# Kernel tuning notes

Measured on AMD Instinct MI355X. Metric: run time of the kernel, lower is better.

Reference implementation:

```python
import jax, jax.numpy as jnp
import numpy as np

EPS = 1e-5

def _quant_w(w):
    # symmetric per-tensor 8-bit weight quantization with straight-through estimator
    s = jnp.max(jnp.abs(w)) / 127.0
    wq = jnp.round(jnp.clip(w / s, -127.0, 127.0)) * s
    return w + jax.lax.stop_gradient(wq - w)

def _adder_conv(x, w, stride):
    # AdderNet conv: out[b,co,ow] = -sum_{cin,k} |x[b,cin,ow*stride+k] - w[co,cin,k]|
    # x: (B, Cin, L), w: (Co, Cin, K)
    B, Cin, L = x.shape
    Co, _, K = w.shape
    Ow = (L - K) // stride + 1
    idx = jnp.arange(Ow)[:, None] * stride + jnp.arange(K)[None, :]      # (Ow, K)
    patches = x[:, :, idx]                                               # (B, Cin, Ow, K)
    diff = jnp.abs(patches[:, None] - w[None, :, :, None, :])            # (B, Co, Cin, Ow, K)
    return -diff.sum(axis=(2, 4))                                        # (B, Co, Ow)

def _bn(x, p):
    # eval-mode BatchNorm; x: (B,C,W), p: (4,C) = [gamma, beta, running_mean, running_var]
    g, b, m, v = p
    return (x - m[:, None]) * (g[:, None] * jax.lax.rsqrt(v[:, None] + EPS)) + b[:, None]

def _bn_params(key, c):
    k1, k2, k3, k4 = jax.random.split(key, 4)
    g = jax.random.uniform(k1, (c,)) + 0.5
    b = 0.1 * jax.random.normal(k2, (c,))
    m = 0.1 * jax.random.normal(k3, (c,))
    v = jax.random.uniform(k4, (c,)) + 0.5
    return jnp.stack([g, b, m, v]).astype(jnp.float32)

def setup_inputs() -> dict:
    key = jax.random.key(0)
    ks = jax.random.split(key, 22)
    B = 8192
    w = lambda k, shp: (0.1 * jax.random.normal(k, shp)).astype(jnp.float32)
    return {
        'x': jax.random.normal(ks[0], (B, 1, 1, 256), dtype=jnp.float32),
        'w_pre1': w(ks[1], (5, 1, 13)),   'bn_pre1': _bn_params(ks[2], 5),
        'w_pre2': w(ks[3], (10, 5, 9)),   'bn_pre2': _bn_params(ks[4], 10),
        'w_r1':   w(ks[5], (10, 10, 1)),  'bn_r1':   _bn_params(ks[6], 10),
        'w_r2':   w(ks[7], (10, 10, 1)),  'bn_r2':   _bn_params(ks[8], 10),
        'w_o1a':  w(ks[9], (70, 140, 1)), 'bn_o1a':  _bn_params(ks[10], 70),
        'w_o1b':  w(ks[11], (30, 70, 1)), 'bn_o1b':  _bn_params(ks[12], 30),
        'w_o1c':  w(ks[13], (1, 30, 1)),  'bn_o1c':  _bn_params(ks[14], 1),
        'w_o2a':  w(ks[15], (70, 140, 1)),'bn_o2a':  _bn_params(ks[16], 70),
        'w_o2b':  w(ks[17], (30, 70, 1)), 'bn_o2b':  _bn_params(ks[18], 30),
        'w_o2c':  w(ks[19], (1, 30, 1)),  'bn_o2c':  _bn_params(ks[20], 1),
    }

def reference(x, w_pre1, bn_pre1, w_pre2, bn_pre2, w_r1, bn_r1, w_r2, bn_r2,
              w_o1a, bn_o1a, w_o1b, bn_o1b, w_o1c, bn_o1c,
              w_o2a, bn_o2a, w_o2b, bn_o2b, w_o2c, bn_o2c):
    relu = jax.nn.relu
    B = x.shape[0]
    h = x.reshape(B, 1, 256)                                  # height dim is 1 -> 1D
    h = relu(_bn(_adder_conv(h, _quant_w(w_pre1), 5), bn_pre1))   # (B,5,49)
    h = relu(_bn(_adder_conv(h, _quant_w(w_pre2), 3), bn_pre2))   # (B,10,14)
    # ResBlock
    t = relu(_bn(_adder_conv(h, _quant_w(w_r1), 1), bn_r1))
    t = _bn(_adder_conv(t, _quant_w(w_r2), 1), bn_r2)
    h = relu(t + h)                                           # (B,10,14)
    f = h.reshape(B, 140, 1)                                  # flatten to channels
    # O1 branch (amplitude-weighted average lifetime)
    a = relu(_bn(_adder_conv(f, _quant_w(w_o1a), 1), bn_o1a))
    a = relu(_bn(_adder_conv(a, _quant_w(w_o1b), 1), bn_o1b))
    a = relu(_bn(_adder_conv(a, _quant_w(w_o1c), 1), bn_o1c))
    tau_amp = a.reshape(-1)                                   # (B,)
    # O2 branch (intensity-weighted average lifetime)
    b = relu(_bn(_adder_conv(f, _quant_w(w_o2a), 1), bn_o2a))
    b = relu(_bn(_adder_conv(b, _quant_w(w_o2b), 1), bn_o2b))
    b = relu(_bn(_adder_conv(b, _quant_w(w_o2c), 1), bn_o2c))
    tau_inten = b.reshape(-1)                                 # (B,)
    return (tau_amp, tau_inten)
```

## Files before the change

kernel.cpp:

```cpp
#include <hip/hip_runtime.h>

#define TPB 256
#define EPB 8
#define H1S 246
#define ES  280

#define WQ1   0
#define WQ2   65
#define WR1Q  515
#define WR2Q  615
#define WCQ   715
#define WSB   779
#define SMALL_N 1253
#define WQAT  1280
#define WQBT  20880

#define SB_P1 0
#define SB_P2 10
#define SB_R1 30
#define SB_R2 50
#define SB_A1 70
#define SB_B1 210
#define SB_C1 270
#define SB_A2 272
#define SB_B2 412
#define SB_C2 472

#define GFOLD(bn, C, OFF)                                                     \
  if (tid < (C)) {                                                            \
    float gg = (bn)[tid], bb = (bn)[(C) + tid];                               \
    float mm = (bn)[2 * (C) + tid], vv = (bn)[3 * (C) + tid];                 \
    float sc = gg / sqrtf(vv + 1e-5f);                                        \
    sbp[(OFF) + tid] = sc;                                                    \
    sbp[(OFF) + (C) + tid] = bb - mm * sc;                                    \
  }

extern "C" __global__ __launch_bounds__(256)
void prep(const float* __restrict__ w1,  const float* __restrict__ bnp1,
          const float* __restrict__ w2,  const float* __restrict__ bnp2,
          const float* __restrict__ wr1, const float* __restrict__ bnr1,
          const float* __restrict__ wr2, const float* __restrict__ bnr2,
          const float* __restrict__ wa1, const float* __restrict__ bna1,
          const float* __restrict__ wb1, const float* __restrict__ bnb1,
          const float* __restrict__ wc1, const float* __restrict__ bnc1,
          const float* __restrict__ wa2, const float* __restrict__ bna2,
          const float* __restrict__ wb2, const float* __restrict__ bnb2,
          const float* __restrict__ wc2, const float* __restrict__ bnc2,
          float* __restrict__ ws)
{
  __shared__ float s_red[4];
  const int tid = threadIdx.x;
  const int b = blockIdx.x;

  if (b == 10) {
    float* sbp = ws + WSB;
    GFOLD(bnp1, 5, SB_P1)  GFOLD(bnp2, 10, SB_P2)
    GFOLD(bnr1, 10, SB_R1) GFOLD(bnr2, 10, SB_R2)
    GFOLD(bna1, 70, SB_A1) GFOLD(bnb1, 30, SB_B1) GFOLD(bnc1, 1, SB_C1)
    GFOLD(bna2, 70, SB_A2) GFOLD(bnb2, 30, SB_B2) GFOLD(bnc2, 1, SB_C2)
    return;
  }

  const float* src; int n; int mode; int rofs; float* dst = ws;
  int ofs = 0;
  switch (b) {
    case 0: src = w1;  ofs = WQ1;      n = 65;   mode = 0; rofs = 0;  break;
    case 1: src = w2;  ofs = WQ2;      n = 450;  mode = 0; rofs = 0;  break;
    case 2: src = wr1; ofs = WR1Q;     n = 100;  mode = 0; rofs = 0;  break;
    case 3: src = wr2; ofs = WR2Q;     n = 100;  mode = 0; rofs = 0;  break;
    case 4: src = wa1; ofs = WQAT;     n = 9800; mode = 1; rofs = 0;  break;
    case 5: src = wb1; ofs = WQBT;     n = 2100; mode = 2; rofs = 0;  break;
    case 6: src = wc1; ofs = WCQ;      n = 30;   mode = 0; rofs = 0;  break;
    case 7: src = wa2; ofs = WQAT;     n = 9800; mode = 1; rofs = 70; break;
    case 8: src = wb2; ofs = WQBT;     n = 2100; mode = 2; rofs = 30; break;
    default:src = wc2; ofs = WCQ + 32; n = 30;   mode = 0; rofs = 0;  break;
  }

  float m = 0.f;
  for (int i = tid; i < n; i += 256) m = fmaxf(m, fabsf(src[i]));
#pragma unroll
  for (int off = 32; off > 0; off >>= 1)
    m = fmaxf(m, __shfl_down(m, off, 64));
  if ((tid & 63) == 0) s_red[tid >> 6] = m;
  __syncthreads();
  m = fmaxf(fmaxf(s_red[0], s_red[1]), fmaxf(s_red[2], s_red[3]));

  float s = m / 127.0f;
  for (int i = tid; i < n; i += 256) {
    float w = src[i];
    float q = rintf(fminf(fmaxf(w / s, -127.f), 127.f)) * s;
    if (mode == 0) {
      dst[ofs + i] = q;
    } else if (mode == 1) {
      int r = i / 140 + rofs, c = i % 140;
      dst[ofs + ((c >> 2) * 140 + r) * 4 + (c & 3)] = q;
    } else {
      int r = i / 70 + rofs, c = i % 70;
      dst[ofs + ((c >> 1) * 60 + r) * 2 + (c & 1)] = q;
    }
  }
}

extern "C" __global__ __launch_bounds__(TPB, 4)
void taunet(const float* __restrict__ x, const float* __restrict__ ws,
            float* __restrict__ out, int B)
{
  __shared__ __align__(16) float s_h1[EPB * H1S];
  __shared__ __align__(16) float s_e[EPB * ES];
  __shared__ __align__(16) float s_small[SMALL_N];

  const int tid = threadIdx.x;
  const int g  = tid >> 5;
  const int l  = tid & 31;
  const int ln = tid & 63;
  const int wv = tid >> 6;
  const int gp = 2 * wv;
  const int elem = blockIdx.x * EPB + g;

  for (int i = ln; i < SMALL_N; i += 64) s_small[i] = ws[i];

  {
    const float4* xb = (const float4*)x;
#pragma unroll
    for (int it = 0; it < 2; ++it) {
      int e = gp + it;
      int ge = blockIdx.x * EPB + e;
      if (ge < B) {
        float4 v = xb[ge * 64 + ln];
        *(float4*)&s_e[e * ES + ln * 4] = v;
      }
    }
  }

  const float* sb = &s_small[WSB];

  {
    const float* xe = &s_e[g * ES];
#pragma unroll
    for (int rep = 0; rep < 2; ++rep) {
      int p = l + 32 * rep;
      bool act = p < 49;
      int ps = act ? p : 0;
      float win[13];
#pragma unroll
      for (int k = 0; k < 13; ++k) win[k] = xe[5 * ps + k];
#pragma unroll
      for (int ci = 0; ci < 5; ++ci) {
        float a0 = 0.f, a1 = 0.f;
#pragma unroll
        for (int k = 0; k < 13; ++k) {
          float d = fabsf(win[k] - ws[WQ1 + ci * 13 + k]);
          if (k & 1) a1 += d; else a0 += d;
        }
        float v = fmaxf(fmaf(-(a0 + a1), ws[WSB + SB_P1 + ci],
                             ws[WSB + SB_P1 + 5 + ci]), 0.f);
        if (act) s_h1[g * H1S + ci * 49 + ps] = v;
      }
    }
  }

  {
    const int ch = l >> 4;
    const int ow16 = l & 15;
    const bool act = ow16 < 14;
    const int ow = act ? ow16 : 0;
    const float* h1b = &s_h1[g * H1S];
    float acc[5] = {0.f, 0.f, 0.f, 0.f, 0.f};
#pragma unroll
    for (int ci = 0; ci < 5; ++ci) {
      float w9[9];
#pragma unroll
      for (int k = 0; k < 9; ++k) w9[k] = h1b[ci * 49 + 3 * ow + k];
#pragma unroll
      for (int c = 0; c < 5; ++c) {
        int co = ch * 5 + c;
        float s0 = 0.f, s1 = 0.f;
#pragma unroll
        for (int k = 0; k < 9; ++k) {
          float d = fabsf(w9[k] - s_small[WQ2 + co * 45 + ci * 9 + k]);
          if (k & 1) s1 += d; else s0 += d;
        }
        acc[c] += s0 + s1;
      }
    }
#pragma unroll
    for (int c = 0; c < 5; ++c) {
      int co = ch * 5 + c;
      float v = fmaxf(fmaf(-acc[c], sb[SB_P2 + co], sb[SB_P2 + 10 + co]), 0.f);
      if (act) s_e[g * ES + co * 14 + ow] = v;
    }
  }

#pragma unroll
  for (int j = 0; j < 5; ++j) {
    int idx = l + 32 * j;
    if (idx < 140) {
      int co = idx / 14, ow = idx % 14;
      float a0 = 0.f, a1 = 0.f;
#pragma unroll
      for (int ci = 0; ci < 10; ++ci) {
        float d = fabsf(s_e[g * ES + ci * 14 + ow] - s_small[WR1Q + co * 10 + ci]);
        if (ci & 1) a1 += d; else a0 += d;
      }
      s_e[g * ES + 140 + idx] =
          fmaxf(fmaf(-(a0 + a1), sb[SB_R1 + co], sb[SB_R1 + 10 + co]), 0.f);
    }
  }

#pragma unroll
  for (int j = 0; j < 5; ++j) {
    int idx = l + 32 * j;
    if (idx < 140) {
      int co = idx / 14, ow = idx % 14;
      float a0 = 0.f, a1 = 0.f;
#pragma unroll
      for (int ci = 0; ci < 10; ++ci) {
        float d = fabsf(s_e[g * ES + 140 + ci * 14 + ow] - s_small[WR2Q + co * 10 + ci]);
        if (ci & 1) a1 += d; else a0 += d;
      }
      float t2 = fmaf(-(a0 + a1), sb[SB_R2 + co], sb[SB_R2 + 10 + co]);
      s_e[g * ES + idx] = fmaxf(t2 + s_e[g * ES + idx], 0.f);
    }
  }

  {
    const float* hb0 = &s_e[gp * ES];
    const float* hb1 = &s_e[(gp + 1) * ES];

    const int r2 = (ln + 128 > 139) ? 139 : ln + 128;
    const int rows[3] = {ln, ln + 64, r2};
    float accA[3][4], accB[3][4];
#pragma unroll
    for (int p = 0; p < 3; ++p)
#pragma unroll
      for (int j = 0; j < 4; ++j) { accA[p][j] = 0.f; accB[p][j] = 0.f; }
#pragma unroll 2
    for (int cb = 0; cb < 35; ++cb) {
      float4 h4 = *(const float4*)&hb0[cb * 4];
      float4 k4 = *(const float4*)&hb1[cb * 4];
#pragma unroll
      for (int p = 0; p < 3; ++p) {
        float4 w4 = *(const float4*)&ws[WQAT + (cb * 140 + rows[p]) * 4];
        accA[p][0] += fabsf(h4.x - w4.x);
        accA[p][1] += fabsf(h4.y - w4.y);
        accA[p][2] += fabsf(h4.z - w4.z);
        accA[p][3] += fabsf(h4.w - w4.w);
        accB[p][0] += fabsf(k4.x - w4.x);
        accB[p][1] += fabsf(k4.y - w4.y);
        accB[p][2] += fabsf(k4.z - w4.z);
        accB[p][3] += fabsf(k4.w - w4.w);
      }
    }
#pragma unroll
    for (int p = 0; p < 3; ++p) {
      int cl = rows[p];
      bool act = (p < 2) || (ln < 12);
      if (act) {
        int co  = cl < 70 ? cl : cl - 70;
        int off = cl < 70 ? SB_A1 : SB_A2;
        float sc = sb[off + co], bi = sb[off + 70 + co];
        float sadA = (accA[p][0] + accA[p][1]) + (accA[p][2] + accA[p][3]);
        float sadB = (accB[p][0] + accB[p][1]) + (accB[p][2] + accB[p][3]);
        s_h1[gp * H1S + cl]       = fmaxf(fmaf(-sadA, sc, bi), 0.f);
        s_h1[(gp + 1) * H1S + cl] = fmaxf(fmaf(-sadB, sc, bi), 0.f);
      }
    }

    {
      bool act = ln < 60;
      int rl = act ? ln : 0;
      int br = rl >= 30;
      int co = br ? rl - 30 : rl;
      const float* h0 = &s_h1[gp * H1S + br * 70];
      const float* h1 = &s_h1[(gp + 1) * H1S + br * 70];
      int off = br ? SB_B2 : SB_B1;
      float a0 = 0.f, a1 = 0.f, b0 = 0.f, b1 = 0.f;
#pragma unroll 8
      for (int ci = 0; ci < 35; ++ci) {
        float2 w2v = *(const float2*)&ws[WQBT + (ci * 60 + rl) * 2];
        a0 += fabsf(h0[2 * ci]     - w2v.x);
        a1 += fabsf(h0[2 * ci + 1] - w2v.y);
        b0 += fabsf(h1[2 * ci]     - w2v.x);
        b1 += fabsf(h1[2 * ci + 1] - w2v.y);
      }
      if (act) {
        float sc = sb[off + co], bi = sb[off + 30 + co];
        s_e[gp * ES + 140 + rl]       = fmaxf(fmaf(-(a0 + a1), sc, bi), 0.f);
        s_e[(gp + 1) * ES + 140 + rl] = fmaxf(fmaf(-(b0 + b1), sc, bi), 0.f);
      }
    }

    for (int br = 0; br < 2; ++br) {
      float d = 0.f;
      if (l < 30)
        d = fabsf(s_e[g * ES + 140 + br * 30 + l] - s_small[WCQ + br * 32 + l]);
#pragma unroll
      for (int off = 16; off > 0; off >>= 1)
        d += __shfl_down(d, off, 32);
      if (l == 0 && elem < B) {
        int sbC = br ? SB_C2 : SB_C1;
        out[br * B + elem] = fmaxf(fmaf(-d, sb[sbC], sb[sbC + 1]), 0.f);
      }
    }
  }
}

extern "C" void kernel_launch(void* const* d_in, const int* in_sizes, int n_in,
                              void* d_out, int out_size, void* d_ws, size_t ws_size,
                              hipStream_t stream) {
  const float* x    = (const float*)d_in[0];
  const float* w1   = (const float*)d_in[1];
  const float* bnp1 = (const float*)d_in[2];
  const float* w2   = (const float*)d_in[3];
  const float* bnp2 = (const float*)d_in[4];
  const float* wr1  = (const float*)d_in[5];
  const float* bnr1 = (const float*)d_in[6];
  const float* wr2  = (const float*)d_in[7];
  const float* bnr2 = (const float*)d_in[8];
  const float* wa1  = (const float*)d_in[9];
  const float* bna1 = (const float*)d_in[10];
  const float* wb1  = (const float*)d_in[11];
  const float* bnb1 = (const float*)d_in[12];
  const float* wc1  = (const float*)d_in[13];
  const float* bnc1 = (const float*)d_in[14];
  const float* wa2  = (const float*)d_in[15];
  const float* bna2 = (const float*)d_in[16];
  const float* wb2  = (const float*)d_in[17];
  const float* bnb2 = (const float*)d_in[18];
  const float* wc2  = (const float*)d_in[19];
  const float* bnc2 = (const float*)d_in[20];

  float* ws = (float*)d_ws;
  int B = in_sizes[0] / 256;
  int blocks = (B + EPB - 1) / EPB;

  hipLaunchKernelGGL(prep, dim3(11), dim3(256), 0, stream,
                     w1, bnp1, w2, bnp2, wr1, bnr1, wr2, bnr2,
                     wa1, bna1, wb1, bnb1, wc1, bnc1,
                     wa2, bna2, wb2, bnb2, wc2, bnc2, ws);

  hipLaunchKernelGGL(taunet, dim3(blocks), dim3(TPB), 0, stream,
                     x, ws, (float*)d_out, B);
}
```

Before: 140.4 us.

## Rebalance third-row SAD work across lanes and vectorize weight prep loads

The first dense layer previously had every lane compute a third row for both elements, which wasted work on lanes 12-63. Now lanes 0-11 handle the tail rows for element A and lanes 12-23 for element B, so each lane does one accumulator set instead of two for that row. The weight-quantization prep kernel, the small-weight shared-memory copy and the second layer's activation reads are also vectorized to float4 and float2. The per-lane branch selecting hb2 adds some divergence and an extra LDS load per iteration, and the float4 reinterpretation of the source arrays assumes they are 16-byte aligned.

```diff
diff --git a/kernel.cpp b/kernel.cpp
--- a/kernel.cpp
+++ b/kernel.cpp
@@ -76,8 +76,16 @@
     default:src = wc2; ofs = WCQ + 32; n = 30;   mode = 0; rofs = 0;  break;
   }
 
+  const int n4 = n >> 2;
+  const float4* s4 = (const float4*)src;
+
   float m = 0.f;
-  for (int i = tid; i < n; i += 256) m = fmaxf(m, fabsf(src[i]));
+  for (int i = tid; i < n4; i += 256) {
+    float4 v = s4[i];
+    m = fmaxf(m, fmaxf(fmaxf(fabsf(v.x), fabsf(v.y)),
+                       fmaxf(fabsf(v.z), fabsf(v.w))));
+  }
+  for (int i = (n4 << 2) + tid; i < n; i += 256) m = fmaxf(m, fabsf(src[i]));
 #pragma unroll
   for (int off = 32; off > 0; off >>= 1)
     m = fmaxf(m, __shfl_down(m, off, 64));
@@ -85,18 +93,41 @@
   __syncthreads();
   m = fmaxf(fmaxf(s_red[0], s_red[1]), fmaxf(s_red[2], s_red[3]));
 
-  float s = m / 127.0f;
-  for (int i = tid; i < n; i += 256) {
-    float w = src[i];
-    float q = rintf(fminf(fmaxf(w / s, -127.f), 127.f)) * s;
-    if (mode == 0) {
-      dst[ofs + i] = q;
-    } else if (mode == 1) {
-      int r = i / 140 + rofs, c = i % 140;
-      dst[ofs + ((c >> 2) * 140 + r) * 4 + (c & 3)] = q;
-    } else {
-      int r = i / 70 + rofs, c = i % 70;
-      dst[ofs + ((c >> 1) * 60 + r) * 2 + (c & 1)] = q;
+  const float s = m / 127.0f;
+  auto qz = [&](float w) {
+    return rintf(fminf(fmaxf(w / s, -127.f), 127.f)) * s;
+  };
+
+  if (mode == 0) {
+    for (int i = tid; i < n4; i += 256) {
+      float4 v = s4[i];
+      int base = 4 * i;
+      dst[ofs + base]     = qz(v.x);
+      dst[ofs + base + 1] = qz(v.y);
+      dst[ofs + base + 2] = qz(v.z);
+      dst[ofs + base + 3] = qz(v.w);
+    }
+    for (int i = (n4 << 2) + tid; i < n; i += 256) dst[ofs + i] = qz(src[i]);
+  } else if (mode == 1) {
+    for (int i = tid; i < n4; i += 256) {
+      float4 v = s4[i];
+      int base = 4 * i;
+      int r = base / 140 + rofs, c = base % 140;
+      float4 q4;
+      q4.x = qz(v.x); q4.y = qz(v.y); q4.z = qz(v.z); q4.w = qz(v.w);
+      *(float4*)&dst[ofs + ((c >> 2) * 140 + r) * 4] = q4;
+    }
+  } else {
+    for (int i = tid; i < n4; i += 256) {
+      float4 v = s4[i];
+      int base = 4 * i;
+      float q[4] = {qz(v.x), qz(v.y), qz(v.z), qz(v.w)};
+#pragma unroll
+      for (int cpt = 0; cpt < 4; ++cpt) {
+        int ii = base + cpt;
+        int r = ii / 70 + rofs, c = ii % 70;
+        dst[ofs + ((c >> 1) * 60 + r) * 2 + (c & 1)] = q[cpt];
+      }
     }
   }
 }
@@ -117,7 +148,12 @@
   const int gp = 2 * wv;
   const int elem = blockIdx.x * EPB + g;
 
-  for (int i = ln; i < SMALL_N; i += 64) s_small[i] = ws[i];
+  {
+    const float4* w4p = (const float4*)ws;
+    for (int i = ln; i < (SMALL_N >> 2); i += 64)
+      *(float4*)&s_small[i * 4] = w4p[i];
+    if (ln == 0) s_small[1252] = ws[1252];
+  }
 
   {
     const float4* xb = (const float4*)x;
@@ -227,20 +263,28 @@
     const float* hb0 = &s_e[gp * ES];
     const float* hb1 = &s_e[(gp + 1) * ES];
 
-    const int r2 = (ln + 128 > 139) ? 139 : ln + 128;
-    const int rows[3] = {ln, ln + 64, r2};
-    float accA[3][4], accB[3][4];
-#pragma unroll
-    for (int p = 0; p < 3; ++p)
+    const int r01[2] = {ln, ln + 64};
+    const bool s2a = ln < 12;
+    const bool s2b = (ln >= 12) && (ln < 24);
+    const int r2 = 128 + (s2a ? ln : (s2b ? ln - 12 : 0));
+    const float* hb2 = s2a ? hb0 : hb1;
+
+    float accA[2][4], accB[2][4], acc2[4];
+#pragma unroll
+    for (int p = 0; p < 2; ++p)
 #pragma unroll
       for (int j = 0; j < 4; ++j) { accA[p][j] = 0.f; accB[p][j] = 0.f; }
+#pragma unroll
+    for (int j = 0; j < 4; ++j) acc2[j] = 0.f;
+
 #pragma unroll 2
     for (int cb = 0; cb < 35; ++cb) {
       float4 h4 = *(const float4*)&hb0[cb * 4];
       float4 k4 = *(const float4*)&hb1[cb * 4];
-#pragma unroll
-      for (int p = 0; p < 3; ++p) {
-        float4 w4 = *(const float4*)&ws[WQAT + (cb * 140 + rows[p]) * 4];
+      float4 p4 = *(const float4*)&hb2[cb * 4];
+#pragma unroll
+      for (int p = 0; p < 2; ++p) {
+        float4 w4 = *(const float4*)&ws[WQAT + (cb * 140 + r01[p]) * 4];
         accA[p][0] += fabsf(h4.x - w4.x);
         accA[p][1] += fabsf(h4.y - w4.y);
         accA[p][2] += fabsf(h4.z - w4.z);
@@ -250,20 +294,30 @@
         accB[p][2] += fabsf(k4.z - w4.z);
         accB[p][3] += fabsf(k4.w - w4.w);
       }
-    }
-#pragma unroll
-    for (int p = 0; p < 3; ++p) {
-      int cl = rows[p];
-      bool act = (p < 2) || (ln < 12);
-      if (act) {
-        int co  = cl < 70 ? cl : cl - 70;
-        int off = cl < 70 ? SB_A1 : SB_A2;
-        float sc = sb[off + co], bi = sb[off + 70 + co];
-        float sadA = (accA[p][0] + accA[p][1]) + (accA[p][2] + accA[p][3]);
-        float sadB = (accB[p][0] + accB[p][1]) + (accB[p][2] + accB[p][3]);
-        s_h1[gp * H1S + cl]       = fmaxf(fmaf(-sadA, sc, bi), 0.f);
-        s_h1[(gp + 1) * H1S + cl] = fmaxf(fmaf(-sadB, sc, bi), 0.f);
-      }
+      float4 w2v = *(const float4*)&ws[WQAT + (cb * 140 + r2) * 4];
+      acc2[0] += fabsf(p4.x - w2v.x);
+      acc2[1] += fabsf(p4.y - w2v.y);
+      acc2[2] += fabsf(p4.z - w2v.z);
+      acc2[3] += fabsf(p4.w - w2v.w);
+    }
+#pragma unroll
+    for (int p = 0; p < 2; ++p) {
+      int cl = r01[p];
+      int co  = cl < 70 ? cl : cl - 70;
+      int off = cl < 70 ? SB_A1 : SB_A2;
+      float sc = sb[off + co], bi = sb[off + 70 + co];
+      float sadA = (accA[p][0] + accA[p][1]) + (accA[p][2] + accA[p][3]);
+      float sadB = (accB[p][0] + accB[p][1]) + (accB[p][2] + accB[p][3]);
+      s_h1[gp * H1S + cl]       = fmaxf(fmaf(-sadA, sc, bi), 0.f);
+      s_h1[(gp + 1) * H1S + cl] = fmaxf(fmaf(-sadB, sc, bi), 0.f);
+    }
+    if (s2a || s2b) {
+      int cl = r2;
+      int co = cl - 70;
+      float sc = sb[SB_A2 + co], bi = sb[SB_A2 + 70 + co];
+      float sad = (acc2[0] + acc2[1]) + (acc2[2] + acc2[3]);
+      int e = s2a ? gp : (gp + 1);
+      s_h1[e * H1S + cl] = fmaxf(fmaf(-sad, sc, bi), 0.f);
     }
 
     {
@@ -278,10 +332,12 @@
 #pragma unroll 8
       for (int ci = 0; ci < 35; ++ci) {
         float2 w2v = *(const float2*)&ws[WQBT + (ci * 60 + rl) * 2];
-        a0 += fabsf(h0[2 * ci]     - w2v.x);
-        a1 += fabsf(h0[2 * ci + 1] - w2v.y);
-        b0 += fabsf(h1[2 * ci]     - w2v.x);
-        b1 += fabsf(h1[2 * ci + 1] - w2v.y);
+        float2 hv0 = *(const float2*)&h0[2 * ci];
+        float2 hv1 = *(const float2*)&h1[2 * ci];
+        a0 += fabsf(hv0.x - w2v.x);
+        a1 += fabsf(hv0.y - w2v.y);
+        b0 += fabsf(hv1.x - w2v.x);
+        b1 += fabsf(hv1.y - w2v.y);
       }
       if (act) {
         float sc = sb[off + co], bi = sb[off + 30 + co];
```

Result: faster. 131.8 us (-6.1%).
